# Kernel optimization log

Measured on AMD Instinct MI355X. Metric: run time of the kernel, lower is better.

Reference implementation:

```python
import jax, jax.numpy as jnp
import numpy as np

B, T, EMB, H, LAT = 8192, 30, 128, 256, 256
DT = 0.03


def _lin(k, din, dout):
    k1, k2 = jax.random.split(k)
    s = 1.0 / np.sqrt(din)
    W = jax.random.uniform(k1, (din, dout), minval=-s, maxval=s, dtype=jnp.float32)
    b = jax.random.uniform(k2, (dout,), minval=-s, maxval=s, dtype=jnp.float32)
    return W, b


def setup_inputs():
    key = jax.random.key(0)
    ks = list(jax.random.split(key, 32))
    inp = {}
    inp['expert_traj'] = jax.random.normal(ks[0], (B, T, 4), dtype=jnp.float32)
    inp['init_state'] = jax.random.normal(ks[1], (B, 4), dtype=jnp.float32)
    inp['eps'] = jax.random.normal(ks[2], (B, LAT), dtype=jnp.float32)
    # encoder params
    inp['enc_emb_W'], inp['enc_emb_b'] = _lin(ks[3], 4, EMB)
    inp['enc_Wih'], inp['enc_bih'] = _lin(ks[4], EMB, 4 * H)
    inp['enc_Whh'], inp['enc_bhh'] = _lin(ks[5], H, 4 * H)
    # mu / log_var MLPs: 4 layers, all HxH since latent==h
    muW, mub, lvW, lvb = [], [], [], []
    for i in range(4):
        W, b = _lin(ks[6 + i], H, H); muW.append(W); mub.append(b)
        W, b = _lin(ks[10 + i], H, H); lvW.append(W); lvb.append(b)
    inp['mu_W'] = jnp.stack(muW); inp['mu_b'] = jnp.stack(mub)
    inp['lv_W'] = jnp.stack(lvW); inp['lv_b'] = jnp.stack(lvb)
    # decoder params
    inp['dec_emb_W'], inp['dec_emb_b'] = _lin(ks[14], 4, EMB)
    inp['dec_init_W'], inp['dec_init_b'] = _lin(ks[15], LAT, H)
    inp['dec_Wih'], inp['dec_bih'] = _lin(ks[16], EMB, 4 * H)
    inp['dec_Whh'], inp['dec_bhh'] = _lin(ks[17], H, 4 * H)
    inp['ctrl_W'], inp['ctrl_b'] = _lin(ks[18], H, 2)
    return inp


def _lstm_cell(x, h, c, Wih, Whh, bih, bhh):
    g = x @ Wih + bih + h @ Whh + bhh            # [B, 4H]
    i, f, gg, o = jnp.split(g, 4, axis=-1)       # torch gate order i,f,g,o
    i = jax.nn.sigmoid(i); f = jax.nn.sigmoid(f)
    gg = jnp.tanh(gg); o = jax.nn.sigmoid(o)
    c = f * c + i * gg
    return o * jnp.tanh(c), c


def reference(expert_traj, init_state, eps,
              enc_emb_W, enc_emb_b, enc_Wih, enc_bih, enc_Whh, enc_bhh,
              mu_W, mu_b, lv_W, lv_b,
              dec_emb_W, dec_emb_b, dec_init_W, dec_init_b,
              dec_Wih, dec_bih, dec_Whh, dec_bhh, ctrl_W, ctrl_b):
    # ---- encoder: relative positions ----
    rel_xy = jnp.concatenate([expert_traj[:, :1, :2],
                              expert_traj[:, 1:, :2] - expert_traj[:, :-1, :2]], axis=1)
    rel = jnp.concatenate([rel_xy, expert_traj[:, :, 2:]], axis=2)  # [B,T,4]
    emb = rel @ enc_emb_W + enc_emb_b                               # [B,T,EMB]
    xs = jnp.swapaxes(emb, 0, 1)                                    # [T,B,EMB]

    def enc_step(carry, x):
        h, c = carry
        h, c = _lstm_cell(x, h, c, enc_Wih, enc_Whh, enc_bih, enc_bhh)
        return (h, c), None
    h0 = jnp.zeros((expert_traj.shape[0], H), dtype=expert_traj.dtype)
    (h_enc, _), _ = jax.lax.scan(enc_step, (h0, h0), xs)

    mu, lv = h_enc, h_enc
    for i in range(4):
        mu = jax.nn.leaky_relu(mu @ mu_W[i] + mu_b[i])
        lv = jax.nn.leaky_relu(lv @ lv_W[i] + lv_b[i])

    # ---- reparameterize + tanh ----
    z = jnp.tanh(eps * jnp.exp(0.5 * lv) + mu)                      # [B,LAT]

    # ---- decoder ----
    hd = z @ dec_init_W + dec_init_b                                # [B,H]

    def dec_step(carry, _):
        h, c, s = carry
        x = s @ dec_emb_W + dec_emb_b
        h, c = _lstm_cell(x, h, c, dec_Wih, dec_Whh, dec_bih, dec_bhh)
        ctrl = h @ ctrl_W + ctrl_b                                  # [B,2]
        pedal = ctrl[:, 0]
        steer = jnp.clip(ctrl[:, 1], -0.5, 0.5)
        x_t, y_t, psi, v = s[:, 0], s[:, 1], s[:, 2], s[:, 3]
        v1 = jnp.clip(v + pedal * DT, 0.0, 10.0)
        psi_dot = jnp.clip(v * jnp.tan(steer) / 2.5, -3.14 / 2, 3.14 / 2)
        s_new = jnp.stack([x_t + v1 * jnp.cos(psi) * DT,
                           y_t + v1 * jnp.sin(psi) * DT,
                           psi + psi_dot * DT,
                           v1], axis=1)
        return (h, c, s_new), s_new

    _, traj = jax.lax.scan(dec_step, (hd, hd, init_state), None, length=T)
    recons = jnp.swapaxes(traj, 0, 1)                               # [B,T,4]
    return recons, expert_traj, mu, lv
```

## Files before the change

### kernel.cpp

```cpp
#include <hip/hip_runtime.h>
#include <math.h>

#define B_ 8192
#define T_ 30
#define H_ 256
#define NG_ 1024
#define DT_ 0.03f
#define RB 32
#define NBLK (B_ / RB)

typedef __attribute__((ext_vector_type(8))) short short8;
typedef __attribute__((ext_vector_type(4))) float f32x4;
typedef __attribute__((ext_vector_type(4))) int i32x4;

__device__ inline float bf2f(unsigned short u) {
    unsigned int x = ((unsigned int)u) << 16;
    return __builtin_bit_cast(float, x);
}
__device__ inline unsigned short f2bf(float f) {
    unsigned int x = __builtin_bit_cast(unsigned int, f);
    return (unsigned short)((x + 0x7FFF + ((x >> 16) & 1)) >> 16);
}
__device__ inline float fast_tanh(float x) {
    float e = __expf(2.f * x);
    return 1.f - 2.f / (e + 1.f);
}
__device__ inline float fast_sigmoid(float x) {
    return 1.f / (1.f + __expf(-x));
}

__global__ void fold_perm_kernel(const float* __restrict__ W1, const float* __restrict__ b1,
                                 const float* __restrict__ W2,
                                 const float* __restrict__ bih, const float* __restrict__ bhh,
                                 float* __restrict__ WxP, float* __restrict__ bfP) {
    __shared__ float sP[4][64];
    const int t63 = threadIdx.x & 63;
    const int kc = threadIdx.x >> 6;
    int o = blockIdx.x * 64 + t63;
    int r = o >> 10;
    int np = o & 1023;
    int bN = np >> 6, g = (np >> 4) & 3, j = np & 15;
    int co = g * 256 + bN * 16 + j;
    const float* w1row = (r < 4) ? (W1 + r * 128) : b1;
    float acc = 0.f;
    #pragma unroll 8
    for (int k = kc * 32; k < kc * 32 + 32; ++k)
        acc = fmaf(w1row[k], W2[k * NG_ + co], acc);
    sP[kc][t63] = acc;
    __syncthreads();
    if (kc == 0) {
        acc = sP[0][t63] + sP[1][t63] + sP[2][t63] + sP[3][t63];
        if (r < 4) WxP[r * NG_ + np] = acc;
        else       bfP[np] = acc + bih[co] + bhh[co];
    }
}

__global__ void prep_pack_i8_kernel(const float* __restrict__ W, signed char* __restrict__ Wpk) {
    int id = blockIdx.x * blockDim.x + threadIdx.x;
    int np = id >> 8, k = id & 255;
    int bN = np >> 6, gg = (np >> 4) & 3, j = np & 15;
    int co = gg * 256 + bN * 16 + j;
    int colgrp = np >> 4, fr = np & 15;
    int k0 = k >> 5, kg = (k >> 3) & 3, e = k & 7;
    float q = rintf(W[(size_t)k * NG_ + co] * 2032.f);
    q = fminf(fmaxf(q, -127.f), 127.f);
    Wpk[colgrp * 4096 + k0 * 512 + kg * 128 + fr * 8 + e] = (signed char)q;
}

__global__ void prep_wt_all_kernel(const float* __restrict__ muW, const float* __restrict__ lvW,
                                   const float* __restrict__ diW, unsigned short* __restrict__ WT9) {
    int m = blockIdx.y;
    const float* src = (m < 4) ? muW + (size_t)m * 65536
                     : (m < 8) ? lvW + (size_t)(m - 4) * 65536
                               : diW;
    int id = blockIdx.x * 256 + threadIdx.x;
    int n = id >> 8, k = id & 255;
    WT9[(size_t)m * 65536 + id] = f2bf(src[k * H_ + n]);
}

__global__ void rel_kernel(const float* __restrict__ traj, float* __restrict__ rel,
                           float4* __restrict__ expert) {
    int id = blockIdx.x * blockDim.x + threadIdx.x;
    if (id >= B_ * T_) return;
    int t = id % T_;
    const float* p = traj + (size_t)id * 4;
    float x = p[0], y = p[1];
    if (t > 0) { x -= p[-4]; y -= p[-3]; }
    float* o = rel + (size_t)id * 4;
    o[0] = x; o[1] = y; o[2] = p[2]; o[3] = p[3];
    expert[id] = ((const float4*)traj)[id];
}

template <int DEC>
__global__ __launch_bounds__(512, 2) void lstm_persist9_kernel(
    const float* __restrict__ rel,
    const signed char* __restrict__ Wpk,
    const float* __restrict__ WxP,
    const float* __restrict__ bfP,
    const float* __restrict__ cInit,
    const unsigned short* __restrict__ hInit,
    const float* __restrict__ initS,
    const float* __restrict__ Wc,
    const float* __restrict__ bc,
    unsigned short* __restrict__ hOut,
    float* __restrict__ recons)
{
    __shared__ signed char hBuf[2][32 * 264];
    __shared__ float wxL[4 * 1024];
    __shared__ float bfL[1024];
    __shared__ float WcL[512];
    __shared__ float sL[RB * 4];
    __shared__ float redL[RB * 8 * 2];

    const int tid = threadIdx.x;
    const int lane = tid & 63;
    const int fr = lane & 15;
    const int kg = lane >> 4;
    const int cg = tid >> 6;
    const int rowBase = blockIdx.x * RB;

    {
        int row = tid >> 4, sb = tid & 15;
        signed char* dst = &hBuf[0][row * 264 + sb * 16];
        if (DEC) {
            const unsigned short* src = hInit + (size_t)(rowBase + row) * 256 + sb * 16;
            #pragma unroll
            for (int i = 0; i < 16; ++i) {
                float h = bf2f(src[i]);
                h = fminf(fmaxf(h, -4.f), 4.f);
                dst[i] = (signed char)(int)rintf(h * 31.75f);
            }
        } else {
            *(long*)(dst) = 0L;
            *(long*)(dst + 8) = 0L;
        }
    }
    #pragma unroll
    for (int w = 0; w < 8; ++w) wxL[tid + w * 512] = WxP[tid + w * 512];
    #pragma unroll
    for (int w = 0; w < 2; ++w) bfL[tid + w * 512] = bfP[tid + w * 512];
    if (DEC) {
        if (tid < 128) *(float4*)(WcL + tid * 4) = *(const float4*)(Wc + tid * 4);
        if (tid < RB)  *(float4*)(sL + tid * 4) = *(const float4*)(initS + (size_t)(rowBase + tid) * 4);
    }
    float bc0 = 0.f, bc1 = 0.f;
    if (DEC && tid < RB) { bc0 = bc[0]; bc1 = bc[1]; }

    float cReg[16];
    #pragma unroll
    for (int sc = 0; sc < 2; ++sc)
        #pragma unroll
        for (int m = 0; m < 2; ++m)
            #pragma unroll
            for (int rr = 0; rr < 4; ++rr) {
                if (DEC) cReg[sc * 8 + m * 4 + rr] =
                    cInit[(size_t)(rowBase + m * 16 + kg * 4 + rr) * 256 + (cg * 2 + sc) * 16 + fr];
                else cReg[sc * 8 + m * 4 + rr] = 0.f;
            }
    float hC[16];

    __syncthreads();

    for (int t = 0; t < T_; ++t) {
        const signed char* rbuf = hBuf[t & 1];
        signed char* wbuf = hBuf[(t + 1) & 1];
        const float dqA = (DEC && t == 0) ? (4.f / 258064.f) : (1.f / 258064.f);

        long afr[2][8];
        #pragma unroll
        for (int m = 0; m < 2; ++m)
            #pragma unroll
            for (int k0 = 0; k0 < 8; ++k0)
                afr[m][k0] = *(const long*)(rbuf + (m * 16 + fr) * 264 + (k0 * 4 + kg) * 8);

        float4 xv[2][4];
        #pragma unroll
        for (int m = 0; m < 2; ++m)
            #pragma unroll
            for (int rr = 0; rr < 4; ++rr) {
                int row = m * 16 + kg * 4 + rr;
                if (DEC) xv[m][rr] = *(const float4*)(sL + row * 4);
                else     xv[m][rr] = *(const float4*)(rel + ((size_t)(rowBase + row) * T_ + t) * 4);
            }

        #pragma unroll
        for (int sc = 0; sc < 2; ++sc) {
            const signed char* wbase = Wpk + (size_t)(cg * 8 + sc * 4) * 4096 + lane * 8;
            long bq[4][4];
            #pragma unroll
            for (int p = 0; p < 4; ++p)
                #pragma unroll
                for (int n = 0; n < 4; ++n)
                    bq[p][n] = *(const long*)(wbase + n * 4096 + p * 512);

            i32x4 acc[2][4] = {};
            #pragma unroll
            for (int k0 = 0; k0 < 8; ++k0) {
                #pragma unroll
                for (int m = 0; m < 2; ++m)
                    #pragma unroll
                    for (int n = 0; n < 4; ++n)
                        acc[m][n] = __builtin_amdgcn_mfma_i32_16x16x32_i8(
                            afr[m][k0], bq[k0 & 3][n], acc[m][n], 0, 0, 0);
                if (k0 + 4 < 8) {
                    #pragma unroll
                    for (int n = 0; n < 4; ++n)
                        bq[k0 & 3][n] = *(const long*)(wbase + n * 4096 + (k0 + 4) * 512);
                }
            }

            const int bn = cg * 2 + sc;
            const int np0 = bn * 64 + fr;
            const int u = bn * 16 + fr;
            float bfv[4], wxv[4][4];
            #pragma unroll
            for (int g = 0; g < 4; ++g) bfv[g] = bfL[np0 + g * 16];
            #pragma unroll
            for (int k = 0; k < 4; ++k)
                #pragma unroll
                for (int g = 0; g < 4; ++g)
                    wxv[k][g] = wxL[k * 1024 + np0 + g * 16];
            #pragma unroll
            for (int m = 0; m < 2; ++m) {
                #pragma unroll
                for (int rr = 0; rr < 4; ++rr) {
                    int row = m * 16 + kg * 4 + rr;
                    float xk[4] = {xv[m][rr].x, xv[m][rr].y, xv[m][rr].z, xv[m][rr].w};
                    float g0 = fmaf((float)acc[m][0][rr], dqA, bfv[0]);
                    float g1 = fmaf((float)acc[m][1][rr], dqA, bfv[1]);
                    float g2 = fmaf((float)acc[m][2][rr], dqA, bfv[2]);
                    float g3 = fmaf((float)acc[m][3][rr], dqA, bfv[3]);
                    #pragma unroll
                    for (int k = 0; k < 4; ++k) {
                        g0 = fmaf(xk[k], wxv[k][0], g0);
                        g1 = fmaf(xk[k], wxv[k][1], g1);
                        g2 = fmaf(xk[k], wxv[k][2], g2);
                        g3 = fmaf(xk[k], wxv[k][3], g3);
                    }
                    float iv = fast_sigmoid(g0);
                    float fv = fast_sigmoid(g1);
                    float gv = fast_tanh(g2);
                    float ov = fast_sigmoid(g3);
                    int ci = sc * 8 + m * 4 + rr;
                    float cn = fv * cReg[ci] + iv * gv;
                    cReg[ci] = cn;
                    float hval = ov * fast_tanh(cn);
                    if (DEC) hC[ci] = hval;
                    wbuf[row * 264 + u] = (signed char)(int)rintf(hval * 127.f);
                }
            }
        }

        if (DEC) {
            float p0[8], p1[8];
            #pragma unroll
            for (int i = 0; i < 8; ++i) { p0[i] = 0.f; p1[i] = 0.f; }
            #pragma unroll
            for (int sc = 0; sc < 2; ++sc) {
                int u = (cg * 2 + sc) * 16 + fr;
                float w0 = WcL[u * 2], w1 = WcL[u * 2 + 1];
                #pragma unroll
                for (int m = 0; m < 2; ++m)
                    #pragma unroll
                    for (int rr = 0; rr < 4; ++rr) {
                        p0[m * 4 + rr] = fmaf(hC[sc * 8 + m * 4 + rr], w0, p0[m * 4 + rr]);
                        p1[m * 4 + rr] = fmaf(hC[sc * 8 + m * 4 + rr], w1, p1[m * 4 + rr]);
                    }
            }
            #pragma unroll
            for (int msk = 1; msk < 16; msk <<= 1)
                #pragma unroll
                for (int i = 0; i < 8; ++i) {
                    p0[i] += __shfl_xor(p0[i], msk);
                    p1[i] += __shfl_xor(p1[i], msk);
                }
            if (fr == 0) {
                #pragma unroll
                for (int m = 0; m < 2; ++m)
                    #pragma unroll
                    for (int rr = 0; rr < 4; ++rr) {
                        int row = m * 16 + kg * 4 + rr;
                        redL[(row * 8 + cg) * 2 + 0] = p0[m * 4 + rr];
                        redL[(row * 8 + cg) * 2 + 1] = p1[m * 4 + rr];
                    }
            }
            __syncthreads();
            if (tid < RB) {
                float q0 = 0.f, q1 = 0.f;
                #pragma unroll
                for (int w = 0; w < 8; ++w) {
                    q0 += redL[(tid * 8 + w) * 2 + 0];
                    q1 += redL[(tid * 8 + w) * 2 + 1];
                }
                float pedal = q0 + bc0;
                float steer = fminf(fmaxf(q1 + bc1, -0.5f), 0.5f);
                float4 sv = *(float4*)(sL + tid * 4);
                float v = sv.w;
                float v1 = fminf(fmaxf(v + pedal * DT_, 0.f), 10.f);
                float pd = fminf(fmaxf(v * tanf(steer) * (1.f / 2.5f), -1.57f), 1.57f);
                float4 ns;
                ns.x = sv.x + v1 * cosf(sv.z) * DT_;
                ns.y = sv.y + v1 * sinf(sv.z) * DT_;
                ns.z = sv.z + pd * DT_;
                ns.w = v1;
                *(float4*)(sL + tid * 4) = ns;
                *(float4*)(recons + ((size_t)(rowBase + tid) * T_ + t) * 4) = ns;
            }
            __syncthreads();
        } else {
            __syncthreads();
        }
    }

    if (!DEC) {
        int row = tid >> 4, sb = tid & 15;
        const signed char* src = &hBuf[T_ & 1][row * 264 + sb * 16];
        unsigned short hv[16];
        #pragma unroll
        for (int i = 0; i < 16; ++i)
            hv[i] = f2bf((float)src[i] * (1.f / 127.f));
        unsigned short* dst = hOut + (size_t)(rowBase + row) * 256 + sb * 16;
        *(short8*)(dst) = *(short8*)(hv);
        *(short8*)(dst + 8) = *(short8*)(hv + 8);
    }
}

__global__ __launch_bounds__(256) void mlp_gemm_kernel(
    const unsigned short* __restrict__ Ain, size_t aZStride,
    const unsigned short* __restrict__ WTb, size_t wZStride,
    const float* __restrict__ b0, const float* __restrict__ b1,
    float* __restrict__ outF, size_t ofZStride,
    unsigned short* __restrict__ outB, size_t obZStride,
    int act)
{
    const int z = blockIdx.z;
    const unsigned short* A  = Ain + (size_t)z * aZStride;
    const unsigned short* WT = WTb + (size_t)z * wZStride;
    const float* bias = z ? b1 : b0;

    __shared__ __align__(16) short sA[64 * 256];
    __shared__ __align__(16) short sBm[64 * 256];
    const int tid = threadIdx.x;
    const int lane = tid & 63;
    const int wr = (tid >> 7) & 1;
    const int wc = (tid >> 6) & 1;
    const int rowBase = blockIdx.x * 64;
    const int nBase = blockIdx.y * 64;

    {
        const unsigned short* gA = A + (size_t)rowBase * 256;
        const unsigned short* gB = WT + (size_t)nBase * 256;
        #pragma unroll
        for (int i = 0; i < 8; ++i) {
            int ch = tid + i * 256;
            int row = ch >> 5, slot = ch & 31;
            float4 va = *(const float4*)(gA + row * 256 + slot * 8);
            float4 vb = *(const float4*)(gB + row * 256 + slot * 8);
            int sl = slot ^ (row & 7);
            *(float4*)(sA + row * 256 + sl * 8) = va;
            *(float4*)(sBm + row * 256 + sl * 8) = vb;
        }
    }
    __syncthreads();

    const int fr = lane & 15;
    const int kg = lane >> 4;
    f32x4 acc[2][2] = {};
    #pragma unroll
    for (int k0 = 0; k0 < 8; ++k0) {
        int kch = k0 * 4 + kg;
        short8 a[2], b[2];
        #pragma unroll
        for (int m = 0; m < 2; ++m) {
            int r = wr * 32 + m * 16 + fr;
            a[m] = *(const short8*)(sA + r * 256 + (kch ^ (r & 7)) * 8);
        }
        #pragma unroll
        for (int n = 0; n < 2; ++n) {
            int r = wc * 32 + n * 16 + fr;
            b[n] = *(const short8*)(sBm + r * 256 + (kch ^ (r & 7)) * 8);
        }
        #pragma unroll
        for (int m = 0; m < 2; ++m)
            #pragma unroll
            for (int n = 0; n < 2; ++n)
                acc[m][n] = __builtin_amdgcn_mfma_f32_16x16x32_bf16(a[m], b[n], acc[m][n], 0, 0, 0);
    }

    #pragma unroll
    for (int m = 0; m < 2; ++m) {
        #pragma unroll
        for (int n = 0; n < 2; ++n) {
            int col = nBase + wc * 32 + n * 16 + fr;
            float bv = bias[col];
            #pragma unroll
            for (int r = 0; r < 4; ++r) {
                int row = rowBase + wr * 32 + m * 16 + kg * 4 + r;
                float v = acc[m][n][r] + bv;
                if (act) v = v > 0.f ? v : 0.01f * v;
                if (outF) outF[(size_t)z * ofZStride + (size_t)row * H_ + col] = v;
                if (outB) outB[(size_t)z * obZStride + (size_t)row * H_ + col] = f2bf(v);
            }
        }
    }
}

__global__ void z_kernel(const float* __restrict__ eps, const float* __restrict__ mu,
                         const float* __restrict__ lv, unsigned short* __restrict__ z) {
    int id = blockIdx.x * blockDim.x + threadIdx.x;
    z[id] = f2bf(tanhf(eps[id] * expf(0.5f * lv[id]) + mu[id]));
}

extern "C" void kernel_launch(void* const* d_in, const int* in_sizes, int n_in,
                              void* d_out, int out_size, void* d_ws, size_t ws_size,
                              hipStream_t stream) {
    (void)in_sizes; (void)n_in; (void)out_size; (void)ws_size;
    const float* traj       = (const float*)d_in[0];
    const float* init_s     = (const float*)d_in[1];
    const float* eps        = (const float*)d_in[2];
    const float* enc_emb_W  = (const float*)d_in[3];
    const float* enc_emb_b  = (const float*)d_in[4];
    const float* enc_Wih    = (const float*)d_in[5];
    const float* enc_bih    = (const float*)d_in[6];
    const float* enc_Whh    = (const float*)d_in[7];
    const float* enc_bhh    = (const float*)d_in[8];
    const float* mu_W       = (const float*)d_in[9];
    const float* mu_b       = (const float*)d_in[10];
    const float* lv_W       = (const float*)d_in[11];
    const float* lv_b       = (const float*)d_in[12];
    const float* dec_emb_W  = (const float*)d_in[13];
    const float* dec_emb_b  = (const float*)d_in[14];
    const float* dec_init_W = (const float*)d_in[15];
    const float* dec_init_b = (const float*)d_in[16];
    const float* dec_Wih    = (const float*)d_in[17];
    const float* dec_bih    = (const float*)d_in[18];
    const float* dec_Whh    = (const float*)d_in[19];
    const float* dec_bhh    = (const float*)d_in[20];
    const float* ctrl_W     = (const float*)d_in[21];
    const float* ctrl_b     = (const float*)d_in[22];

    float* out = (float*)d_out;
    float* recons = out;
    float* expert = out + (size_t)B_ * T_ * 4;
    float* mu_out = expert + (size_t)B_ * T_ * 4;
    float* lv_out = mu_out + (size_t)B_ * H_;

    float* ws = (float*)d_ws;
    size_t o = 0;
    float* rel = ws + o;  o += (size_t)B_ * T_ * 4;
    signed char* WpkE = (signed char*)(ws + o); o += NG_ * H_ / 4;
    signed char* WpkD = (signed char*)(ws + o); o += NG_ * H_ / 4;
    unsigned short* WT9  = (unsigned short*)(ws + o); o += 9 * H_ * H_ / 2;
    float* WxPE = ws + o; o += 4 * NG_;
    float* WxPD = ws + o; o += 4 * NG_;
    float* bfPE = ws + o; o += NG_;
    float* bfPD = ws + o; o += NG_;
    unsigned short* hEnc = (unsigned short*)(ws + o); o += (size_t)B_ * H_ / 2;
    unsigned short* tbA  = (unsigned short*)(ws + o); o += (size_t)B_ * H_;
    unsigned short* tbB  = (unsigned short*)(ws + o); o += (size_t)B_ * H_;
    float* cInit = ws + o; o += (size_t)B_ * H_;
    unsigned short* hInit = (unsigned short*)(ws + o); o += (size_t)B_ * H_ / 2;

    fold_perm_kernel<<<80, 256, 0, stream>>>(enc_emb_W, enc_emb_b, enc_Wih, enc_bih, enc_bhh, WxPE, bfPE);
    fold_perm_kernel<<<80, 256, 0, stream>>>(dec_emb_W, dec_emb_b, dec_Wih, dec_bih, dec_bhh, WxPD, bfPD);
    prep_pack_i8_kernel<<<1024, 256, 0, stream>>>(enc_Whh, WpkE);
    prep_pack_i8_kernel<<<1024, 256, 0, stream>>>(dec_Whh, WpkD);
    prep_wt_all_kernel<<<dim3(256, 9), 256, 0, stream>>>(mu_W, lv_W, dec_init_W, WT9);
    rel_kernel<<<(B_ * T_ + 255) / 256, 256, 0, stream>>>(traj, rel, (float4*)expert);

    lstm_persist9_kernel<0><<<NBLK, 512, 0, stream>>>(
        rel, WpkE, WxPE, bfPE, nullptr, nullptr, nullptr, nullptr, nullptr, hEnc, nullptr);

    dim3 gridM2(B_ / 64, H_ / 64, 2);
    size_t BH = (size_t)B_ * H_;
    mlp_gemm_kernel<<<gridM2, 256, 0, stream>>>(hEnc, 0, WT9 + 0 * 65536, (size_t)4 * 65536,
                                                mu_b + 0,   lv_b + 0,   nullptr, 0, tbA, BH, 1);
    mlp_gemm_kernel<<<gridM2, 256, 0, stream>>>(tbA, BH, WT9 + 1 * 65536, (size_t)4 * 65536,
                                                mu_b + 256, lv_b + 256, nullptr, 0, tbB, BH, 1);
    mlp_gemm_kernel<<<gridM2, 256, 0, stream>>>(tbB, BH, WT9 + 2 * 65536, (size_t)4 * 65536,
                                                mu_b + 512, lv_b + 512, nullptr, 0, tbA, BH, 1);
    mlp_gemm_kernel<<<gridM2, 256, 0, stream>>>(tbA, BH, WT9 + 3 * 65536, (size_t)4 * 65536,
                                                mu_b + 768, lv_b + 768, mu_out, BH, nullptr, 0, 1);

    z_kernel<<<B_ * H_ / 256, 256, 0, stream>>>(eps, mu_out, lv_out, tbB);
    dim3 gridM1(B_ / 64, H_ / 64, 1);
    mlp_gemm_kernel<<<gridM1, 256, 0, stream>>>(tbB, 0, WT9 + 8 * 65536, 0,
                                                dec_init_b, dec_init_b, cInit, 0, hInit, 0, 0);

    lstm_persist9_kernel<1><<<NBLK, 512, 0, stream>>>(
        nullptr, WpkD, WxPD, bfPD, cInit, hInit, init_s, ctrl_W, ctrl_b, nullptr, recons);
}
```

Baseline: 939.9 us.

## Halve LSTM rows per block to 16 and raise occupancy to four blocks

Reduces the batch rows handled per persistent LSTM block from 32 to 16, doubling the grid to 512 blocks and dropping the second M-tile of MFMAs. Register arrays for the cell state, h values and A fragments shrink, and launch bounds now ask for 4 blocks per CU instead of 2. The aim is more wavefronts in flight to hide latency in the recurrent step. The trade-off is that each block streams the full int8 recurrent weights from global memory for only half as many rows, which doubles weight traffic per row, and per-block setup (the wx/bias LDS fill) is repeated twice as often.

```diff
diff --git a/kernel.cpp b/kernel.cpp
--- a/kernel.cpp
+++ b/kernel.cpp
@@ -6,7 +6,7 @@
 #define H_ 256
 #define NG_ 1024
 #define DT_ 0.03f
-#define RB 32
+#define RB 16
 #define NBLK (B_ / RB)
 
 typedef __attribute__((ext_vector_type(8))) short short8;
@@ -92,7 +92,7 @@
 }
 
 template <int DEC>
-__global__ __launch_bounds__(512, 2) void lstm_persist9_kernel(
+__global__ __launch_bounds__(512, 4) void lstm_persist10_kernel(
     const float* __restrict__ rel,
     const signed char* __restrict__ Wpk,
     const float* __restrict__ WxP,
@@ -105,7 +105,7 @@
     unsigned short* __restrict__ hOut,
     float* __restrict__ recons)
 {
-    __shared__ signed char hBuf[2][32 * 264];
+    __shared__ signed char hBuf[2][16 * 264];
     __shared__ float wxL[4 * 1024];
     __shared__ float bfL[1024];
     __shared__ float WcL[512];
@@ -120,19 +120,18 @@
     const int rowBase = blockIdx.x * RB;
 
     {
-        int row = tid >> 4, sb = tid & 15;
-        signed char* dst = &hBuf[0][row * 264 + sb * 16];
+        int row = tid >> 5, sb = tid & 31;
+        signed char* dst = &hBuf[0][row * 264 + sb * 8];
         if (DEC) {
-            const unsigned short* src = hInit + (size_t)(rowBase + row) * 256 + sb * 16;
-            #pragma unroll
-            for (int i = 0; i < 16; ++i) {
+            const unsigned short* src = hInit + (size_t)(rowBase + row) * 256 + sb * 8;
+            #pragma unroll
+            for (int i = 0; i < 8; ++i) {
                 float h = bf2f(src[i]);
                 h = fminf(fmaxf(h, -4.f), 4.f);
                 dst[i] = (signed char)(int)rintf(h * 31.75f);
             }
         } else {
             *(long*)(dst) = 0L;
-            *(long*)(dst + 8) = 0L;
         }
     }
     #pragma unroll
@@ -146,18 +145,16 @@
     float bc0 = 0.f, bc1 = 0.f;
     if (DEC && tid < RB) { bc0 = bc[0]; bc1 = bc[1]; }
 
-    float cReg[16];
+    float cReg[8];
     #pragma unroll
     for (int sc = 0; sc < 2; ++sc)
         #pragma unroll
-        for (int m = 0; m < 2; ++m)
-            #pragma unroll
-            for (int rr = 0; rr < 4; ++rr) {
-                if (DEC) cReg[sc * 8 + m * 4 + rr] =
-                    cInit[(size_t)(rowBase + m * 16 + kg * 4 + rr) * 256 + (cg * 2 + sc) * 16 + fr];
-                else cReg[sc * 8 + m * 4 + rr] = 0.f;
-            }
-    float hC[16];
+        for (int rr = 0; rr < 4; ++rr) {
+            if (DEC) cReg[sc * 4 + rr] =
+                cInit[(size_t)(rowBase + kg * 4 + rr) * 256 + (cg * 2 + sc) * 16 + fr];
+            else cReg[sc * 4 + rr] = 0.f;
+        }
+    float hC[8];
 
     __syncthreads();
 
@@ -166,22 +163,18 @@
         signed char* wbuf = hBuf[(t + 1) & 1];
         const float dqA = (DEC && t == 0) ? (4.f / 258064.f) : (1.f / 258064.f);
 
-        long afr[2][8];
-        #pragma unroll
-        for (int m = 0; m < 2; ++m)
-            #pragma unroll
-            for (int k0 = 0; k0 < 8; ++k0)
-                afr[m][k0] = *(const long*)(rbuf + (m * 16 + fr) * 264 + (k0 * 4 + kg) * 8);
-
-        float4 xv[2][4];
-        #pragma unroll
-        for (int m = 0; m < 2; ++m)
-            #pragma unroll
-            for (int rr = 0; rr < 4; ++rr) {
-                int row = m * 16 + kg * 4 + rr;
-                if (DEC) xv[m][rr] = *(const float4*)(sL + row * 4);
-                else     xv[m][rr] = *(const float4*)(rel + ((size_t)(rowBase + row) * T_ + t) * 4);
-            }
+        long afr[8];
+        #pragma unroll
+        for (int k0 = 0; k0 < 8; ++k0)
+            afr[k0] = *(const long*)(rbuf + fr * 264 + (k0 * 4 + kg) * 8);
+
+        float4 xv[4];
+        #pragma unroll
+        for (int rr = 0; rr < 4; ++rr) {
+            int row = kg * 4 + rr;
+            if (DEC) xv[rr] = *(const float4*)(sL + row * 4);
+            else     xv[rr] = *(const float4*)(rel + ((size_t)(rowBase + row) * T_ + t) * 4);
+        }
 
         #pragma unroll
         for (int sc = 0; sc < 2; ++sc) {
@@ -193,15 +186,13 @@
                 for (int n = 0; n < 4; ++n)
                     bq[p][n] = *(const long*)(wbase + n * 4096 + p * 512);
 
-            i32x4 acc[2][4] = {};
+            i32x4 acc[4] = {};
             #pragma unroll
             for (int k0 = 0; k0 < 8; ++k0) {
                 #pragma unroll
-                for (int m = 0; m < 2; ++m)
-                    #pragma unroll
-                    for (int n = 0; n < 4; ++n)
-                        acc[m][n] = __builtin_amdgcn_mfma_i32_16x16x32_i8(
-                            afr[m][k0], bq[k0 & 3][n], acc[m][n], 0, 0, 0);
+                for (int n = 0; n < 4; ++n)
+                    acc[n] = __builtin_amdgcn_mfma_i32_16x16x32_i8(
+                        afr[k0], bq[k0 & 3][n], acc[n], 0, 0, 0);
                 if (k0 + 4 < 8) {
                     #pragma unroll
                     for (int n = 0; n < 4; ++n)
@@ -221,68 +212,61 @@
                 for (int g = 0; g < 4; ++g)
                     wxv[k][g] = wxL[k * 1024 + np0 + g * 16];
             #pragma unroll
-            for (int m = 0; m < 2; ++m) {
-                #pragma unroll
-                for (int rr = 0; rr < 4; ++rr) {
-                    int row = m * 16 + kg * 4 + rr;
-                    float xk[4] = {xv[m][rr].x, xv[m][rr].y, xv[m][rr].z, xv[m][rr].w};
-                    float g0 = fmaf((float)acc[m][0][rr], dqA, bfv[0]);
-                    float g1 = fmaf((float)acc[m][1][rr], dqA, bfv[1]);
-                    float g2 = fmaf((float)acc[m][2][rr], dqA, bfv[2]);
-                    float g3 = fmaf((float)acc[m][3][rr], dqA, bfv[3]);
-                    #pragma unroll
-                    for (int k = 0; k < 4; ++k) {
-                        g0 = fmaf(xk[k], wxv[k][0], g0);
-                        g1 = fmaf(xk[k], wxv[k][1], g1);
-                        g2 = fmaf(xk[k], wxv[k][2], g2);
-                        g3 = fmaf(xk[k], wxv[k][3], g3);
-                    }
-                    float iv = fast_sigmoid(g0);
-                    float fv = fast_sigmoid(g1);
-                    float gv = fast_tanh(g2);
-                    float ov = fast_sigmoid(g3);
-                    int ci = sc * 8 + m * 4 + rr;
-                    float cn = fv * cReg[ci] + iv * gv;
-                    cReg[ci] = cn;
-                    float hval = ov * fast_tanh(cn);
-                    if (DEC) hC[ci] = hval;
-                    wbuf[row * 264 + u] = (signed char)(int)rintf(hval * 127.f);
-                }
+            for (int rr = 0; rr < 4; ++rr) {
+                int row = kg * 4 + rr;
+                float xk[4] = {xv[rr].x, xv[rr].y, xv[rr].z, xv[rr].w};
+                float g0 = fmaf((float)acc[0][rr], dqA, bfv[0]);
+                float g1 = fmaf((float)acc[1][rr], dqA, bfv[1]);
+                float g2 = fmaf((float)acc[2][rr], dqA, bfv[2]);
+                float g3 = fmaf((float)acc[3][rr], dqA, bfv[3]);
+                #pragma unroll
+                for (int k = 0; k < 4; ++k) {
+                    g0 = fmaf(xk[k], wxv[k][0], g0);
+                    g1 = fmaf(xk[k], wxv[k][1], g1);
+                    g2 = fmaf(xk[k], wxv[k][2], g2);
+                    g3 = fmaf(xk[k], wxv[k][3], g3);
+                }
+                float iv = fast_sigmoid(g0);
+                float fv = fast_sigmoid(g1);
+                float gv = fast_tanh(g2);
+                float ov = fast_sigmoid(g3);
+                int ci = sc * 4 + rr;
+                float cn = fv * cReg[ci] + iv * gv;
+                cReg[ci] = cn;
+                float hval = ov * fast_tanh(cn);
+                if (DEC) hC[ci] = hval;
+                wbuf[row * 264 + u] = (signed char)(int)rintf(hval * 127.f);
             }
         }
 
         if (DEC) {
-            float p0[8], p1[8];
-            #pragma unroll
-            for (int i = 0; i < 8; ++i) { p0[i] = 0.f; p1[i] = 0.f; }
+            float p0[4], p1[4];
+            #pragma unroll
+            for (int i = 0; i < 4; ++i) { p0[i] = 0.f; p1[i] = 0.f; }
             #pragma unroll
             for (int sc = 0; sc < 2; ++sc) {
                 int u = (cg * 2 + sc) * 16 + fr;
                 float w0 = WcL[u * 2], w1 = WcL[u * 2 + 1];
                 #pragma unroll
-                for (int m = 0; m < 2; ++m)
-                    #pragma unroll
-                    for (int rr = 0; rr < 4; ++rr) {
-                        p0[m * 4 + rr] = fmaf(hC[sc * 8 + m * 4 + rr], w0, p0[m * 4 + rr]);
-                        p1[m * 4 + rr] = fmaf(hC[sc * 8 + m * 4 + rr], w1, p1[m * 4 + rr]);
-                    }
+                for (int rr = 0; rr < 4; ++rr) {
+                    p0[rr] = fmaf(hC[sc * 4 + rr], w0, p0[rr]);
+                    p1[rr] = fmaf(hC[sc * 4 + rr], w1, p1[rr]);
+                }
             }
             #pragma unroll
             for (int msk = 1; msk < 16; msk <<= 1)
                 #pragma unroll
-                for (int i = 0; i < 8; ++i) {
+                for (int i = 0; i < 4; ++i) {
                     p0[i] += __shfl_xor(p0[i], msk);
                     p1[i] += __shfl_xor(p1[i], msk);
                 }
             if (fr == 0) {
                 #pragma unroll
-                for (int m = 0; m < 2; ++m)
-                    #pragma unroll
-                    for (int rr = 0; rr < 4; ++rr) {
-                        int row = m * 16 + kg * 4 + rr;
-                        redL[(row * 8 + cg) * 2 + 0] = p0[m * 4 + rr];
-                        redL[(row * 8 + cg) * 2 + 1] = p1[m * 4 + rr];
-                    }
+                for (int rr = 0; rr < 4; ++rr) {
+                    int row = kg * 4 + rr;
+                    redL[(row * 8 + cg) * 2 + 0] = p0[rr];
+                    redL[(row * 8 + cg) * 2 + 1] = p1[rr];
+                }
             }
             __syncthreads();
             if (tid < RB) {
@@ -313,15 +297,13 @@
     }
 
     if (!DEC) {
-        int row = tid >> 4, sb = tid & 15;
-        const signed char* src = &hBuf[T_ & 1][row * 264 + sb * 16];
-        unsigned short hv[16];
-        #pragma unroll
-        for (int i = 0; i < 16; ++i)
+        int row = tid >> 5, seg = tid & 31;
+        const signed char* src = &hBuf[T_ & 1][row * 264 + seg * 8];
+        unsigned short hv[8];
+        #pragma unroll
+        for (int i = 0; i < 8; ++i)
             hv[i] = f2bf((float)src[i] * (1.f / 127.f));
-        unsigned short* dst = hOut + (size_t)(rowBase + row) * 256 + sb * 16;
-        *(short8*)(dst) = *(short8*)(hv);
-        *(short8*)(dst + 8) = *(short8*)(hv + 8);
+        *(short8*)(hOut + (size_t)(rowBase + row) * 256 + seg * 8) = *(short8*)(hv);
     }
 }
 
@@ -468,7 +450,7 @@
     prep_wt_all_kernel<<<dim3(256, 9), 256, 0, stream>>>(mu_W, lv_W, dec_init_W, WT9);
     rel_kernel<<<(B_ * T_ + 255) / 256, 256, 0, stream>>>(traj, rel, (float4*)expert);
 
-    lstm_persist9_kernel<0><<<NBLK, 512, 0, stream>>>(
+    lstm_persist10_kernel<0><<<NBLK, 512, 0, stream>>>(
         rel, WpkE, WxPE, bfPE, nullptr, nullptr, nullptr, nullptr, nullptr, hEnc, nullptr);
 
     dim3 gridM2(B_ / 64, H_ / 64, 2);
@@ -487,6 +469,6 @@
     mlp_gemm_kernel<<<gridM1, 256, 0, stream>>>(tbB, 0, WT9 + 8 * 65536, 0,
                                                 dec_init_b, dec_init_b, cInit, 0, hInit, 0, 0);
 
-    lstm_persist9_kernel<1><<<NBLK, 512, 0, stream>>>(
+    lstm_persist10_kernel<1><<<NBLK, 512, 0, stream>>>(
         nullptr, WpkD, WxPD, bfPD, cInit, hInit, init_s, ctrl_W, ctrl_b, nullptr, recons);
 }
```

Result: slower. 1.257 ms (+33.8%).

## Keep recurrent int8 weights resident in registers across LSTM timesteps

Applied to the files above, without the earlier changes.

Each thread loads its slice of the packed int8 recurrent weight matrix (64 longs) into registers once before the time loop, instead of reloading it from global memory every timestep. The loop is reordered so the M tile is outermost, and the control projection is accumulated inline, which removes the hC array. This targets per-step global and L2 weight traffic, at the cost of about 128 extra VGPRs per thread. That risks spilling under the 512-thread, 2-block launch bounds.

```diff
diff --git a/kernel.cpp b/kernel.cpp
--- a/kernel.cpp
+++ b/kernel.cpp
@@ -92,7 +92,7 @@
 }
 
 template <int DEC>
-__global__ __launch_bounds__(512, 2) void lstm_persist9_kernel(
+__global__ __launch_bounds__(512, 2) void lstm_persist11_kernel(
     const float* __restrict__ rel,
     const signed char* __restrict__ Wpk,
     const float* __restrict__ WxP,
@@ -119,6 +119,18 @@
     const int cg = tid >> 6;
     const int rowBase = blockIdx.x * RB;
 
+    long wB[2][4][8];
+    {
+        const signed char* wbase = Wpk + (size_t)cg * 8 * 4096 + lane * 8;
+        #pragma unroll
+        for (int sc = 0; sc < 2; ++sc)
+            #pragma unroll
+            for (int n = 0; n < 4; ++n)
+                #pragma unroll
+                for (int k0 = 0; k0 < 8; ++k0)
+                    wB[sc][n][k0] = *(const long*)(wbase + (sc * 4 + n) * 4096 + k0 * 512);
+    }
+
     {
         int row = tid >> 4, sb = tid & 15;
         signed char* dst = &hBuf[0][row * 264 + sb * 16];
@@ -157,7 +169,6 @@
                     cInit[(size_t)(rowBase + m * 16 + kg * 4 + rr) * 256 + (cg * 2 + sc) * 16 + fr];
                 else cReg[sc * 8 + m * 4 + rr] = 0.f;
             }
-    float hC[16];
 
     __syncthreads();
 
@@ -166,70 +177,58 @@
         signed char* wbuf = hBuf[(t + 1) & 1];
         const float dqA = (DEC && t == 0) ? (4.f / 258064.f) : (1.f / 258064.f);
 
-        long afr[2][8];
-        #pragma unroll
-        for (int m = 0; m < 2; ++m)
+        float p0[8], p1[8];
+        if (DEC) {
+            #pragma unroll
+            for (int i = 0; i < 8; ++i) { p0[i] = 0.f; p1[i] = 0.f; }
+        }
+
+        #pragma unroll
+        for (int m = 0; m < 2; ++m) {
+            long afr[8];
             #pragma unroll
             for (int k0 = 0; k0 < 8; ++k0)
-                afr[m][k0] = *(const long*)(rbuf + (m * 16 + fr) * 264 + (k0 * 4 + kg) * 8);
-
-        float4 xv[2][4];
-        #pragma unroll
-        for (int m = 0; m < 2; ++m)
+                afr[k0] = *(const long*)(rbuf + (m * 16 + fr) * 264 + (k0 * 4 + kg) * 8);
+            float4 xv[4];
             #pragma unroll
             for (int rr = 0; rr < 4; ++rr) {
                 int row = m * 16 + kg * 4 + rr;
-                if (DEC) xv[m][rr] = *(const float4*)(sL + row * 4);
-                else     xv[m][rr] = *(const float4*)(rel + ((size_t)(rowBase + row) * T_ + t) * 4);
-            }
-
-        #pragma unroll
-        for (int sc = 0; sc < 2; ++sc) {
-            const signed char* wbase = Wpk + (size_t)(cg * 8 + sc * 4) * 4096 + lane * 8;
-            long bq[4][4];
-            #pragma unroll
-            for (int p = 0; p < 4; ++p)
-                #pragma unroll
-                for (int n = 0; n < 4; ++n)
-                    bq[p][n] = *(const long*)(wbase + n * 4096 + p * 512);
-
-            i32x4 acc[2][4] = {};
-            #pragma unroll
-            for (int k0 = 0; k0 < 8; ++k0) {
-                #pragma unroll
-                for (int m = 0; m < 2; ++m)
+                if (DEC) xv[rr] = *(const float4*)(sL + row * 4);
+                else     xv[rr] = *(const float4*)(rel + ((size_t)(rowBase + row) * T_ + t) * 4);
+            }
+
+            #pragma unroll
+            for (int sc = 0; sc < 2; ++sc) {
+                i32x4 acc[4] = {};
+                #pragma unroll
+                for (int k0 = 0; k0 < 8; ++k0) {
+                    acc[0] = __builtin_amdgcn_mfma_i32_16x16x32_i8(afr[k0], wB[sc][0][k0], acc[0], 0, 0, 0);
+                    acc[1] = __builtin_amdgcn_mfma_i32_16x16x32_i8(afr[k0], wB[sc][1][k0], acc[1], 0, 0, 0);
+                    acc[2] = __builtin_amdgcn_mfma_i32_16x16x32_i8(afr[k0], wB[sc][2][k0], acc[2], 0, 0, 0);
+                    acc[3] = __builtin_amdgcn_mfma_i32_16x16x32_i8(afr[k0], wB[sc][3][k0], acc[3], 0, 0, 0);
+                }
+
+                const int bn = cg * 2 + sc;
+                const int np0 = bn * 64 + fr;
+                const int u = bn * 16 + fr;
+                float w0 = 0.f, w1 = 0.f;
+                if (DEC) { w0 = WcL[u * 2]; w1 = WcL[u * 2 + 1]; }
+                float bfv[4], wxv[4][4];
+                #pragma unroll
+                for (int g = 0; g < 4; ++g) bfv[g] = bfL[np0 + g * 16];
+                #pragma unroll
+                for (int k = 0; k < 4; ++k)
                     #pragma unroll
-                    for (int n = 0; n < 4; ++n)
-                        acc[m][n] = __builtin_amdgcn_mfma_i32_16x16x32_i8(
-                            afr[m][k0], bq[k0 & 3][n], acc[m][n], 0, 0, 0);
-                if (k0 + 4 < 8) {
-                    #pragma unroll
-                    for (int n = 0; n < 4; ++n)
-                        bq[k0 & 3][n] = *(const long*)(wbase + n * 4096 + (k0 + 4) * 512);
-                }
-            }
-
-            const int bn = cg * 2 + sc;
-            const int np0 = bn * 64 + fr;
-            const int u = bn * 16 + fr;
-            float bfv[4], wxv[4][4];
-            #pragma unroll
-            for (int g = 0; g < 4; ++g) bfv[g] = bfL[np0 + g * 16];
-            #pragma unroll
-            for (int k = 0; k < 4; ++k)
-                #pragma unroll
-                for (int g = 0; g < 4; ++g)
-                    wxv[k][g] = wxL[k * 1024 + np0 + g * 16];
-            #pragma unroll
-            for (int m = 0; m < 2; ++m) {
+                    for (int g = 0; g < 4; ++g)
+                        wxv[k][g] = wxL[k * 1024 + np0 + g * 16];
                 #pragma unroll
                 for (int rr = 0; rr < 4; ++rr) {
                     int row = m * 16 + kg * 4 + rr;
-                    float xk[4] = {xv[m][rr].x, xv[m][rr].y, xv[m][rr].z, xv[m][rr].w};
-                    float g0 = fmaf((float)acc[m][0][rr], dqA, bfv[0]);
-                    float g1 = fmaf((float)acc[m][1][rr], dqA, bfv[1]);
-                    float g2 = fmaf((float)acc[m][2][rr], dqA, bfv[2]);
-                    float g3 = fmaf((float)acc[m][3][rr], dqA, bfv[3]);
+                    float xk[4] = {xv[rr].x, xv[rr].y, xv[rr].z, xv[rr].w};
+                    float g0 = fmaf((float)acc[0][rr], dqA, bfv[0]);
+                    float g1 = fmaf((float)acc[1][rr], dqA, bfv[1]);
+                    float g2 = fmaf((float)acc[2][rr], dqA, bfv[2]);
+                    float g3 = fmaf((float)acc[3][rr], dqA, bfv[3]);
                     #pragma unroll
                     for (int k = 0; k < 4; ++k) {
                         g0 = fmaf(xk[k], wxv[k][0], g0);
@@ -245,28 +244,16 @@
                     float cn = fv * cReg[ci] + iv * gv;
                     cReg[ci] = cn;
                     float hval = ov * fast_tanh(cn);
-                    if (DEC) hC[ci] = hval;
+                    if (DEC) {
+                        p0[m * 4 + rr] = fmaf(hval, w0, p0[m * 4 + rr]);
+                        p1[m * 4 + rr] = fmaf(hval, w1, p1[m * 4 + rr]);
+                    }
                     wbuf[row * 264 + u] = (signed char)(int)rintf(hval * 127.f);
                 }
             }
         }
 
         if (DEC) {
-            float p0[8], p1[8];
-            #pragma unroll
-            for (int i = 0; i < 8; ++i) { p0[i] = 0.f; p1[i] = 0.f; }
-            #pragma unroll
-            for (int sc = 0; sc < 2; ++sc) {
-                int u = (cg * 2 + sc) * 16 + fr;
-                float w0 = WcL[u * 2], w1 = WcL[u * 2 + 1];
-                #pragma unroll
-                for (int m = 0; m < 2; ++m)
-                    #pragma unroll
-                    for (int rr = 0; rr < 4; ++rr) {
-                        p0[m * 4 + rr] = fmaf(hC[sc * 8 + m * 4 + rr], w0, p0[m * 4 + rr]);
-                        p1[m * 4 + rr] = fmaf(hC[sc * 8 + m * 4 + rr], w1, p1[m * 4 + rr]);
-                    }
-            }
             #pragma unroll
             for (int msk = 1; msk < 16; msk <<= 1)
                 #pragma unroll
@@ -468,7 +455,7 @@
     prep_wt_all_kernel<<<dim3(256, 9), 256, 0, stream>>>(mu_W, lv_W, dec_init_W, WT9);
     rel_kernel<<<(B_ * T_ + 255) / 256, 256, 0, stream>>>(traj, rel, (float4*)expert);
 
-    lstm_persist9_kernel<0><<<NBLK, 512, 0, stream>>>(
+    lstm_persist11_kernel<0><<<NBLK, 512, 0, stream>>>(
         rel, WpkE, WxPE, bfPE, nullptr, nullptr, nullptr, nullptr, nullptr, hEnc, nullptr);
 
     dim3 gridM2(B_ / 64, H_ / 64, 2);
@@ -487,6 +474,6 @@
     mlp_gemm_kernel<<<gridM1, 256, 0, stream>>>(tbB, 0, WT9 + 8 * 65536, 0,
                                                 dec_init_b, dec_init_b, cInit, 0, hInit, 0, 0);
 
-    lstm_persist9_kernel<1><<<NBLK, 512, 0, stream>>>(
+    lstm_persist11_kernel<1><<<NBLK, 512, 0, stream>>>(
         nullptr, WpkD, WxPD, bfPD, cInit, hInit, init_s, ctrl_W, ctrl_b, nullptr, recons);
 }
```

After: 1.082 ms. 15.1% more time.
